# Kernel tuning notes

Measured on AMD Instinct MI355X. Metric: run time of the kernel, lower is better.

Reference implementation:

```python
import jax, jax.numpy as jnp
import numpy as np

IDIM = 512
HDIM = 1024
CDIM = 128  # part_size; topk uses k = 2*CDIM (share=True)
B, T = 16, 4096


def _multihot(idx, n):
    """idx: [B, T, K] int32 -> [B, T, n] float 0/1 multi-hot.
    Matches one_hot(idx, n).float().sum(-2); topk indices are unique so add==set."""
    b, t, k = idx.shape
    rows = jnp.arange(b * t)[:, None]
    m = jnp.zeros((b * t, n), jnp.float32).at[rows, idx.reshape(-1, k)].add(1.0)
    return m.reshape(b, t, n)


def setup_inputs() -> dict:
    key = jax.random.key(0)
    ks = jax.random.split(key, 12)
    inp = {}
    inp["x"] = jax.random.normal(ks[0], (B, T, IDIM), jnp.float32)
    inp["mask_prev"] = (jax.random.uniform(ks[1], (B, T, HDIM)) < 0.1).astype(jnp.float32)

    def lin(k, i, o):
        return jax.random.normal(k, (i, o), jnp.float32) * (1.0 / np.sqrt(i))

    dims_e = [IDIM, 512, 512, 512, HDIM]
    dims_d = [HDIM, 512, 512, 512, IDIM]
    for i in range(4):
        inp[f"e_w{i}"] = lin(ks[2 + i], dims_e[i], dims_e[i + 1])
        inp[f"e_b{i}"] = jnp.zeros((dims_e[i + 1],), jnp.float32)
        inp[f"d_w{i}"] = lin(ks[6 + i], dims_d[i], dims_d[i + 1])
        inp[f"d_b{i}"] = jnp.zeros((dims_d[i + 1],), jnp.float32)
    return inp


def _mlp(x, ws, bs):
    for w, b in zip(ws[:-1], bs[:-1]):
        x = jax.nn.relu(x @ w + b)
    return x @ ws[-1] + bs[-1]


def reference(x, mask_prev,
              e_w0, e_b0, e_w1, e_b1, e_w2, e_b2, e_w3, e_b3,
              d_w0, d_b0, d_w1, d_b1, d_w2, d_b2, d_w3, d_b3):
    h = _mlp(x, [e_w0, e_w1, e_w2, e_w3], [e_b0, e_b1, e_b2, e_b3])  # [B,T,HDIM]

    # hidden_exclude_activation (mask_prev is not None branch)
    h = jnp.where(mask_prev > 0, jnp.float32(0.0), h)  # h[mask_prev.byte()] = 0
    energy = h * h
    _, idx = jax.lax.top_k(energy, 2 * CDIM)            # sorted desc, like torch.topk
    mask_cur_share = _multihot(idx, HDIM)               # top 2*cdim multi-hot
    # h.masked_fill(~mask_cur_share, 0): keep only the shared top-2*cdim energies
    h = h * mask_cur_share

    # decoder
    out = _mlp(h, [d_w0, d_w1, d_w2, d_w3], [d_b0, d_b1, d_b2, d_b3])  # [B,T,IDIM]
    return out
```

## Files before the change

### kernel.cpp

```cpp
#include <hip/hip_runtime.h>

constexpr int NTOK  = 16 * 4096;
constexpr int KSEL  = 256;
constexpr int UCAP  = 8192;
constexpr int NCHNK = 2;
constexpr int UCAPT = UCAP * NCHNK;

using short8 = __attribute__((ext_vector_type(8))) short;
using ush4   = __attribute__((ext_vector_type(4))) unsigned short;
using f32x4  = __attribute__((ext_vector_type(4))) float;

__device__ inline unsigned short bf16_rne(float x) {
    unsigned u = __float_as_uint(x);
    unsigned r = u + 0x7fffu + ((u >> 16) & 1u);
    return (unsigned short)(r >> 16);
}
__device__ inline float bf16_f32(unsigned short h) {
    return __uint_as_float((unsigned)h << 16);
}

__device__ inline void gload_lds16(const unsigned short* g, unsigned short* l) {
    __builtin_amdgcn_global_load_lds(
        (const __attribute__((address_space(1))) void*)g,
        (__attribute__((address_space(3))) void*)l, 16, 0, 0);
}

__global__ __launch_bounds__(256)
void wsplit_t(const float* __restrict__ W, unsigned short* __restrict__ WhT,
              unsigned short* __restrict__ WlT, int K, int M)
{
    __shared__ float tile[32][33];
    const int tid = threadIdx.x;
    const int tx = tid & 31, ty = tid >> 5;
    const int m0 = blockIdx.x * 32, k0 = blockIdx.y * 32;
#pragma unroll
    for (int i = 0; i < 4; ++i)
        tile[ty + 8 * i][tx] = W[(size_t)(k0 + ty + 8 * i) * M + m0 + tx];
    __syncthreads();
#pragma unroll
    for (int i = 0; i < 4; ++i) {
        int m = ty + 8 * i;
        float v = tile[tx][m];
        unsigned short hh = bf16_rne(v);
        unsigned short ll = bf16_rne(v - bf16_f32(hh));
        WhT[(size_t)(m0 + m) * K + k0 + tx] = hh;
        WlT[(size_t)(m0 + m) * K + k0 + tx] = ll;
    }
}

template<int K, int RELU, int OUT_SPLIT>
__global__ __launch_bounds__(256)
void gemm_s(const unsigned short* __restrict__ A,
            const unsigned short* __restrict__ WhT,
            const unsigned short* __restrict__ WlT,
            const float* __restrict__ bias,
            void* Cp, int M, const float* __restrict__ mask)
{
    __shared__ __align__(16) unsigned short sAh[128 * 32];
    __shared__ __align__(16) unsigned short sAl[128 * 32];
    __shared__ __align__(16) unsigned short sBh[128 * 32];
    __shared__ __align__(16) unsigned short sBl[128 * 32];

    const int tid = threadIdx.x;
    const int lane = tid & 63, wid = tid >> 6;
    const int quad = lane >> 4, l16 = lane & 15;

    const int gridX = gridDim.x;
    int nwg = gridX * gridDim.y;
    int bid = blockIdx.y * gridX + blockIdx.x;
    int cpx = nwg >> 3;
    int swz = (bid & 7) * cpx + (bid >> 3);
    const int rowBase = (swz / gridX) * 128;
    const int colBase = (swz % gridX) * 128;

    const int wr = (wid & 1) * 64, wc = (wid >> 1) * 64;

    const int srl = lane >> 2;
    const int sq  = lane & 3;

    f32x4 acc[4][4];
#pragma unroll
    for (int i = 0; i < 4; ++i)
#pragma unroll
        for (int j = 0; j < 4; ++j)
            acc[i][j] = (f32x4){0.f, 0.f, 0.f, 0.f};

    for (int k0 = 0; k0 < K; k0 += 32) {
        __syncthreads();
#pragma unroll
        for (int i16 = 0; i16 < 2; ++i16) {
            const int row = wid * 32 + i16 * 16 + srl;
            const int qs = sq ^ ((row >> 1) & 3);
            const unsigned short* gAh = A  + (size_t)(rowBase + row) * (2 * K) + k0 + qs * 8;
            const unsigned short* gBh = WhT + (size_t)(colBase + row) * K + k0 + qs * 8;
            const unsigned short* gBl = WlT + (size_t)(colBase + row) * K + k0 + qs * 8;
            unsigned short* dst = (unsigned short*)0;
            const int dbase = (wid * 32 + i16 * 16) * 32;
            gload_lds16(gAh,     &sAh[dbase]);
            gload_lds16(gAh + K, &sAl[dbase]);
            gload_lds16(gBh,     &sBh[dbase]);
            gload_lds16(gBl,     &sBl[dbase]);
            (void)dst;
        }
        asm volatile("s_waitcnt vmcnt(0)" ::: "memory");
        __syncthreads();

        short8 ah[4], al[4], bh[4], bl[4];
#pragma unroll
        for (int t4 = 0; t4 < 4; ++t4) {
            const int ra = wr + t4 * 16 + l16;
            const int rb = wc + t4 * 16 + l16;
            const int ca = (quad ^ ((ra >> 1) & 3)) * 8;
            const int cb = (quad ^ ((rb >> 1) & 3)) * 8;
            ah[t4] = *(const short8*)&sAh[ra * 32 + ca];
            al[t4] = *(const short8*)&sAl[ra * 32 + ca];
            bh[t4] = *(const short8*)&sBh[rb * 32 + cb];
            bl[t4] = *(const short8*)&sBl[rb * 32 + cb];
        }
#pragma unroll
        for (int rt = 0; rt < 4; ++rt)
#pragma unroll
            for (int ct = 0; ct < 4; ++ct) {
                acc[rt][ct] = __builtin_amdgcn_mfma_f32_16x16x32_bf16(ah[rt], bh[ct], acc[rt][ct], 0, 0, 0);
                acc[rt][ct] = __builtin_amdgcn_mfma_f32_16x16x32_bf16(al[rt], bh[ct], acc[rt][ct], 0, 0, 0);
                acc[rt][ct] = __builtin_amdgcn_mfma_f32_16x16x32_bf16(ah[rt], bl[ct], acc[rt][ct], 0, 0, 0);
            }
    }

#pragma unroll
    for (int ct = 0; ct < 4; ++ct) {
        int col = colBase + wc + ct * 16 + l16;
        float bc = bias[col];
#pragma unroll
        for (int rt = 0; rt < 4; ++rt)
#pragma unroll
            for (int r = 0; r < 4; ++r) {
                int row = rowBase + wr + rt * 16 + quad * 4 + r;
                float v = acc[rt][ct][r] + bc;
                if (RELU) v = fmaxf(v, 0.f);
                if (mask) { if (mask[(size_t)row * M + col] > 0.f) v = 0.f; }
                if constexpr (OUT_SPLIT) {
                    unsigned short* Cs = (unsigned short*)Cp;
                    unsigned short hh = bf16_rne(v);
                    unsigned short ll = bf16_rne(v - bf16_f32(hh));
                    Cs[(size_t)row * (2 * M) + col]     = hh;
                    Cs[(size_t)row * (2 * M) + M + col] = ll;
                } else {
                    ((float*)Cp)[(size_t)row * M + col] = v;
                }
            }
    }
}

template<int K, int RELU, int OUT_SPLIT>
__global__ __launch_bounds__(256)
void gemm_u(const float* __restrict__ Af, const unsigned short* __restrict__ WhT,
            const unsigned short* __restrict__ WlT, const float* __restrict__ bias,
            void* Cp, int M, const float* __restrict__ mask)
{
    __shared__ __align__(16) unsigned short sAh[128 * 40];
    __shared__ __align__(16) unsigned short sAl[128 * 40];
    __shared__ __align__(16) unsigned short sBh[128 * 40];
    __shared__ __align__(16) unsigned short sBl[128 * 40];

    const int tid = threadIdx.x;
    const int lane = tid & 63, wid = tid >> 6;
    const int quad = lane >> 4, l16 = lane & 15;

    const int gridX = gridDim.x;
    int nwg = gridX * gridDim.y;
    int bid = blockIdx.y * gridX + blockIdx.x;
    int cpx = nwg >> 3;
    int swz = (bid & 7) * cpx + (bid >> 3);
    const int rowBase = (swz / gridX) * 128;
    const int colBase = (swz % gridX) * 128;

    const int wr = (wid & 1) * 64, wc = (wid >> 1) * 64;
    const int sr = tid >> 1;
    const int sk = (tid & 1) * 16;

    f32x4 acc[4][4];
#pragma unroll
    for (int i = 0; i < 4; ++i)
#pragma unroll
        for (int j = 0; j < 4; ++j)
            acc[i][j] = (f32x4){0.f, 0.f, 0.f, 0.f};

    for (int k0 = 0; k0 < K; k0 += 32) {
        const float* ap = &Af[(size_t)(rowBase + sr) * K + k0 + sk];
        float4 a0 = *(const float4*)ap;
        float4 a1 = *(const float4*)(ap + 4);
        float4 a2 = *(const float4*)(ap + 8);
        float4 a3 = *(const float4*)(ap + 12);
        const unsigned short* whp = &WhT[(size_t)(colBase + sr) * K + k0 + sk];
        const unsigned short* wlp = &WlT[(size_t)(colBase + sr) * K + k0 + sk];
        short8 wh0 = *(const short8*)whp;
        short8 wh1 = *(const short8*)(whp + 8);
        short8 wl0 = *(const short8*)wlp;
        short8 wl1 = *(const short8*)(wlp + 8);

        float f[16] = {a0.x, a0.y, a0.z, a0.w, a1.x, a1.y, a1.z, a1.w,
                       a2.x, a2.y, a2.z, a2.w, a3.x, a3.y, a3.z, a3.w};
        unsigned short __align__(16) hs[16], ls[16];
#pragma unroll
        for (int j = 0; j < 16; ++j) {
            hs[j] = bf16_rne(f[j]);
            ls[j] = bf16_rne(f[j] - bf16_f32(hs[j]));
        }

        __syncthreads();
        *(short8*)&sAh[sr * 40 + sk]     = *(short8*)&hs[0];
        *(short8*)&sAh[sr * 40 + sk + 8] = *(short8*)&hs[8];
        *(short8*)&sAl[sr * 40 + sk]     = *(short8*)&ls[0];
        *(short8*)&sAl[sr * 40 + sk + 8] = *(short8*)&ls[8];
        *(short8*)&sBh[sr * 40 + sk]     = wh0;
        *(short8*)&sBh[sr * 40 + sk + 8] = wh1;
        *(short8*)&sBl[sr * 40 + sk]     = wl0;
        *(short8*)&sBl[sr * 40 + sk + 8] = wl1;
        __syncthreads();

        short8 ah[4], al[4], bh[4], bl[4];
#pragma unroll
        for (int t4 = 0; t4 < 4; ++t4) {
            ah[t4] = *(const short8*)&sAh[(wr + t4 * 16 + l16) * 40 + quad * 8];
            al[t4] = *(const short8*)&sAl[(wr + t4 * 16 + l16) * 40 + quad * 8];
            bh[t4] = *(const short8*)&sBh[(wc + t4 * 16 + l16) * 40 + quad * 8];
            bl[t4] = *(const short8*)&sBl[(wc + t4 * 16 + l16) * 40 + quad * 8];
        }
#pragma unroll
        for (int rt = 0; rt < 4; ++rt)
#pragma unroll
            for (int ct = 0; ct < 4; ++ct) {
                acc[rt][ct] = __builtin_amdgcn_mfma_f32_16x16x32_bf16(ah[rt], bh[ct], acc[rt][ct], 0, 0, 0);
                acc[rt][ct] = __builtin_amdgcn_mfma_f32_16x16x32_bf16(al[rt], bh[ct], acc[rt][ct], 0, 0, 0);
                acc[rt][ct] = __builtin_amdgcn_mfma_f32_16x16x32_bf16(ah[rt], bl[ct], acc[rt][ct], 0, 0, 0);
            }
    }

#pragma unroll
    for (int ct = 0; ct < 4; ++ct) {
        int col = colBase + wc + ct * 16 + l16;
        float bc = bias[col];
#pragma unroll
        for (int rt = 0; rt < 4; ++rt)
#pragma unroll
            for (int r = 0; r < 4; ++r) {
                int row = rowBase + wr + rt * 16 + quad * 4 + r;
                float v = acc[rt][ct][r] + bc;
                if (RELU) v = fmaxf(v, 0.f);
                if (mask) { if (mask[(size_t)row * M + col] > 0.f) v = 0.f; }
                if constexpr (OUT_SPLIT) {
                    unsigned short* Cs = (unsigned short*)Cp;
                    unsigned short hh = bf16_rne(v);
                    unsigned short ll = bf16_rne(v - bf16_f32(hh));
                    Cs[(size_t)row * (2 * M) + col]     = hh;
                    Cs[(size_t)row * (2 * M) + M + col] = ll;
                } else {
                    ((float*)Cp)[(size_t)row * M + col] = v;
                }
            }
    }
}

__global__ __launch_bounds__(256)
void topk_pass1(const float* h, unsigned short* hsplit, int* __restrict__ meta)
{
    const int t = blockIdx.x, tid = threadIdx.x;
    const int lane = tid & 63, wid = tid >> 6;

    __shared__ unsigned hist[256];
    __shared__ unsigned wsum[4];
    __shared__ unsigned dmx[4];
    __shared__ unsigned s_prefix;
    __shared__ int s_need;

    float4 hv = ((const float4*)(h + (size_t)t * 1024))[tid];
    float v[4] = {hv.x, hv.y, hv.z, hv.w};
    unsigned u[4];
#pragma unroll
    for (int j = 0; j < 4; ++j) u[j] = __float_as_uint(v[j] * v[j]);

    if (tid == 0) { s_prefix = 0u; s_need = KSEL; }
    __syncthreads();

    for (int p = 3; p >= 0; --p) {
        unsigned pref = s_prefix;
        int need = s_need;
        hist[tid] = 0u;
        __syncthreads();
#pragma unroll
        for (int j = 0; j < 4; ++j) {
            bool match = (p == 3) || ((u[j] >> (8 * (p + 1))) == (pref >> (8 * (p + 1))));
            if (match) atomicAdd(&hist[(u[j] >> (8 * p)) & 255u], 1u);
        }
        __syncthreads();
        unsigned x = hist[tid];
        unsigned s = x;
#pragma unroll
        for (int off = 1; off < 64; off <<= 1) {
            unsigned o = __shfl_down(s, off);
            if (lane + off < 64) s += o;
        }
        if (lane == 0) wsum[wid] = s;
        __syncthreads();
        unsigned above = 0;
        for (int w = wid + 1; w < 4; ++w) above += wsum[w];
        unsigned incl = s + above;
        unsigned excl = incl - x;
        if (incl >= (unsigned)need && excl < (unsigned)need) {
            s_prefix = pref | ((unsigned)tid << (8 * p));
            s_need = need - (int)excl;
        }
        __syncthreads();
    }
    const unsigned tau = s_prefix;

    unsigned cg = 0, ce = 0;
#pragma unroll
    for (int j = 0; j < 4; ++j) {
        cg += (u[j] > tau) ? 1u : 0u;
        ce += (u[j] == tau) ? 1u : 0u;
    }
    unsigned packed = (cg << 16) | ce;
    unsigned ps = packed;
#pragma unroll
    for (int off = 1; off < 64; off <<= 1) {
        unsigned o = __shfl_up(ps, off);
        if (lane >= off) ps += o;
    }
    if (lane == 63) wsum[wid] = ps;
    __syncthreads();
    unsigned below = 0;
    for (int w = 0; w < wid; ++w) below += wsum[w];
    unsigned total = wsum[0] + wsum[1] + wsum[2] + wsum[3];
    unsigned incl = ps + below;
    int need_eq = KSEL - (int)(total >> 16);
    int eq_base = (int)((incl - packed) & 0xffffu);

    bool kp[4];
    {
        int r = 0;
#pragma unroll
        for (int j = 0; j < 4; ++j) {
            if (u[j] > tau) kp[j] = true;
            else if (u[j] == tau) { kp[j] = (eq_base + r) < need_eq; ++r; }
            else kp[j] = false;
        }
    }

    unsigned dmax = 0;
#pragma unroll
    for (int j = 0; j < 4; ++j) if (!kp[j] && u[j] > dmax) dmax = u[j];
#pragma unroll
    for (int off = 32; off > 0; off >>= 1) {
        unsigned o = __shfl_xor(dmax, off);
        if (o > dmax) dmax = o;
    }
    if (lane == 0) dmx[wid] = dmax;
    __syncthreads();
    if (tid == 0) {
        unsigned lo = dmx[0];
        for (int w = 1; w < 4; ++w) if (dmx[w] > lo) lo = dmx[w];
        float tauf = __uint_as_float(tau);
        float lof  = __uint_as_float(lo);
        if (tauf - lof <= fmaf(tauf, 4e-4f, 4e-5f)) {
            int slot = atomicAdd(&meta[0], 1);
            if (slot < UCAPT) meta[1 + slot] = t;
        }
    }

    unsigned short hs[4], ls[4];
#pragma unroll
    for (int j = 0; j < 4; ++j) {
        float ov = kp[j] ? v[j] : 0.f;
        hs[j] = bf16_rne(ov);
        ls[j] = bf16_rne(ov - bf16_f32(hs[j]));
    }
    size_t base = (size_t)t * 2048 + 4 * tid;
    *(ush4*)&hsplit[base]        = (ush4){hs[0], hs[1], hs[2], hs[3]};
    *(ush4*)&hsplit[base + 1024] = (ush4){ls[0], ls[1], ls[2], ls[3]};
}

__global__ __launch_bounds__(256)
void gather_x(const float* __restrict__ x, double* __restrict__ a64,
              const int* __restrict__ meta, int chunk)
{
    int cnt = meta[0]; if (cnt > UCAPT) cnt = UCAPT;
    int g = chunk * UCAP + blockIdx.x;
    if (g >= cnt) return;
    int tok = meta[1 + g];
    const float* src = &x[(size_t)tok * 512];
    double* dst = &a64[(size_t)blockIdx.x * 512];
    for (int i = threadIdx.x; i < 512; i += 256) dst[i] = (double)src[i];
}

template<int K, int RELU, int MASKED>
__global__ __launch_bounds__(256)
void gemm_f64(const double* __restrict__ A, const float* __restrict__ W,
              const float* __restrict__ bias, double* __restrict__ Cd,
              int M, const int* __restrict__ meta, const float* __restrict__ mp,
              int chunk)
{
    int cnt = meta[0]; if (cnt > UCAPT) cnt = UCAPT;
    int cloc = cnt - chunk * UCAP;
    if (cloc < 0) cloc = 0; if (cloc > UCAP) cloc = UCAP;
    const int rowBase = blockIdx.y * 64;
    if (rowBase >= cloc) return;
    const int colBase = blockIdx.x * 64;

    __shared__ double sA[16][65];
    __shared__ double sW[16][65];
    const int tid = threadIdx.x;
    const int tx = tid & 15, ty = tid >> 4;
    const int lr = tid & 63;
    const int lk4 = (tid >> 6) * 4;
    const int wk = tid >> 4;
    const int wc = (tid & 15) * 4;

    double acc[4][4] = {};

    for (int k0 = 0; k0 < K; k0 += 16) {
        const double* ap = &A[(size_t)(rowBase + lr) * K + k0 + lk4];
        double a0 = ap[0], a1 = ap[1], a2 = ap[2], a3 = ap[3];
        float4 wv = *(const float4*)&W[(size_t)(k0 + wk) * M + colBase + wc];
        __syncthreads();
        sA[lk4 + 0][lr] = a0; sA[lk4 + 1][lr] = a1;
        sA[lk4 + 2][lr] = a2; sA[lk4 + 3][lr] = a3;
        sW[wk][wc + 0] = (double)wv.x; sW[wk][wc + 1] = (double)wv.y;
        sW[wk][wc + 2] = (double)wv.z; sW[wk][wc + 3] = (double)wv.w;
        __syncthreads();
#pragma unroll
        for (int k = 0; k < 16; ++k) {
            double av[4], wl[4];
#pragma unroll
            for (int i = 0; i < 4; ++i) av[i] = sA[k][ty * 4 + i];
#pragma unroll
            for (int i = 0; i < 4; ++i) wl[i] = sW[k][tx * 4 + i];
#pragma unroll
            for (int a = 0; a < 4; ++a)
#pragma unroll
                for (int b = 0; b < 4; ++b)
                    acc[a][b] = fma(av[a], wl[b], acc[a][b]);
        }
    }

#pragma unroll
    for (int a = 0; a < 4; ++a) {
        int row = rowBase + ty * 4 + a;
        if (row >= cloc) continue;
        int tok = MASKED ? meta[1 + chunk * UCAP + row] : 0;
#pragma unroll
        for (int b = 0; b < 4; ++b) {
            int col = colBase + tx * 4 + b;
            double vv = acc[a][b] + (double)bias[col];
            if (RELU) vv = vv > 0.0 ? vv : 0.0;
            if (MASKED) { if (mp[(size_t)tok * 1024 + col] > 0.f) vv = 0.0; }
            Cd[(size_t)row * M + col] = vv;
        }
    }
}

__global__ __launch_bounds__(256)
void topk_pass2(const double* __restrict__ h64, unsigned short* __restrict__ hsplit,
                const int* __restrict__ meta, int chunk)
{
    int cnt = meta[0]; if (cnt > UCAPT) cnt = UCAPT;
    int g = chunk * UCAP + blockIdx.x;
    if (g >= cnt) return;
    int tok = meta[1 + g];

    __shared__ double se[1024];
    __shared__ unsigned short si[1024];
    __shared__ unsigned char keep[1024];
    const int tid = threadIdx.x;
    const double* row = &h64[(size_t)blockIdx.x * 1024];

#pragma unroll
    for (int t = 0; t < 4; ++t) {
        int i = tid + t * 256;
        double v = row[i];
        se[i] = v * v;
        si[i] = (unsigned short)i;
        keep[i] = 0;
    }
    __syncthreads();

    for (int ksz = 2; ksz <= 1024; ksz <<= 1) {
        for (int j = ksz >> 1; j > 0; j >>= 1) {
#pragma unroll
            for (int t = 0; t < 4; ++t) {
                int i = tid + t * 256;
                int p = i ^ j;
                if (p > i) {
                    double ei = se[i], ep = se[p];
                    unsigned short ii = si[i], ip = si[p];
                    bool later = !((ei > ep) || (ei == ep && ii < ip));
                    bool dir = ((i & ksz) == 0);
                    if (later == dir) {
                        se[i] = ep; se[p] = ei;
                        si[i] = ip; si[p] = ii;
                    }
                }
            }
            __syncthreads();
        }
    }

    keep[si[tid]] = 1;
    __syncthreads();

#pragma unroll
    for (int t = 0; t < 4; ++t) {
        int i = tid + t * 256;
        float vv = keep[i] ? (float)row[i] : 0.f;
        unsigned short hh = bf16_rne(vv);
        unsigned short ll = bf16_rne(vv - bf16_f32(hh));
        hsplit[(size_t)tok * 2048 + i]        = hh;
        hsplit[(size_t)tok * 2048 + 1024 + i] = ll;
    }
}

extern "C" void kernel_launch(void* const* d_in, const int* in_sizes, int n_in,
                              void* d_out, int out_size, void* d_ws, size_t ws_size,
                              hipStream_t stream)
{
    (void)n_in; (void)out_size; (void)ws_size;

    const float* x  = (const float*)d_in[0];
    const float* mp = (const float*)d_in[1];

    const float *ew[4], *eb[4], *dw[4], *db[4];
    bool interleaved = (in_sizes[4] == 1024 * 512);
    for (int i = 0; i < 4; ++i) {
        if (interleaved) {
            ew[i] = (const float*)d_in[2 + 4 * i];
            eb[i] = (const float*)d_in[3 + 4 * i];
            dw[i] = (const float*)d_in[4 + 4 * i];
            db[i] = (const float*)d_in[5 + 4 * i];
        } else {
            ew[i] = (const float*)d_in[2 + 2 * i];
            eb[i] = (const float*)d_in[3 + 2 * i];
            dw[i] = (const float*)d_in[10 + 2 * i];
            db[i] = (const float*)d_in[11 + 2 * i];
        }
    }

    char* ws = (char*)d_ws;
    char* ob = (char*)d_out;
    const size_t MB = 1024 * 1024;

    unsigned short* S1 = (unsigned short*)(ws);
    unsigned short* S2 = (unsigned short*)(ws + 128 * MB);
    unsigned short* S3 = (unsigned short*)(ws + 256 * MB);
    float*          hF = (float*)(ws);
    unsigned short* Hs = (unsigned short*)(ws);
    unsigned short* D1 = (unsigned short*)(ws + 256 * MB);
    unsigned short* D2 = (unsigned short*)(ws);
    unsigned short* D3 = (unsigned short*)(ws + 128 * MB);
    float*          out = (float*)d_out;

    unsigned short* p0 = (unsigned short*)ob;
    unsigned short* EW0h = p0 + 0;        unsigned short* EW0l = p0 + 262144;
    unsigned short* EW1h = p0 + 524288;   unsigned short* EW1l = p0 + 786432;
    unsigned short* EW2h = p0 + 1048576;  unsigned short* EW2l = p0 + 1310720;
    unsigned short* EW3h = p0 + 1572864;  unsigned short* EW3l = p0 + 2097152;
    unsigned short* W0h  = p0 + 2621440;  unsigned short* W0l  = p0 + 3145728;
    unsigned short* W1h  = p0 + 3670016;  unsigned short* W1l  = p0 + 3932160;
    unsigned short* W2h  = p0 + 4194304;  unsigned short* W2l  = p0 + 4456448;
    int* meta = (int*)(ob + 16 * MB);

    unsigned short* W3h = (unsigned short*)(ws + 256 * MB);
    unsigned short* W3l = W3h + 262144;

    double* a64 = (double*)(ws + 256 * MB);
    double* b64 = (double*)(ws + 288 * MB);
    double* h64 = (double*)(ws + 320 * MB);

    dim3 blk(256);

    wsplit_t<<<dim3(16, 16), blk, 0, stream>>>(ew[0], EW0h, EW0l, 512, 512);
    wsplit_t<<<dim3(16, 16), blk, 0, stream>>>(ew[1], EW1h, EW1l, 512, 512);
    wsplit_t<<<dim3(16, 16), blk, 0, stream>>>(ew[2], EW2h, EW2l, 512, 512);
    wsplit_t<<<dim3(32, 16), blk, 0, stream>>>(ew[3], EW3h, EW3l, 512, 1024);
    wsplit_t<<<dim3(16, 32), blk, 0, stream>>>(dw[0], W0h,  W0l,  1024, 512);
    wsplit_t<<<dim3(16, 16), blk, 0, stream>>>(dw[1], W1h,  W1l,  512, 512);
    wsplit_t<<<dim3(16, 16), blk, 0, stream>>>(dw[2], W2h,  W2l,  512, 512);
    hipMemsetAsync(meta, 0, sizeof(int), stream);

    dim3 ge(4, NTOK / 128), ge4(8, NTOK / 128);
    gemm_u<512, 1, 1><<<ge,  blk, 0, stream>>>(x,  EW0h, EW0l, eb[0], S1, 512,  nullptr);
    gemm_s<512, 1, 1><<<ge,  blk, 0, stream>>>(S1, EW1h, EW1l, eb[1], S2, 512,  nullptr);
    gemm_s<512, 1, 1><<<ge,  blk, 0, stream>>>(S2, EW2h, EW2l, eb[2], S3, 512,  nullptr);
    gemm_s<512, 0, 0><<<ge4, blk, 0, stream>>>(S3, EW3h, EW3l, eb[3], hF, 1024, mp);

    topk_pass1<<<dim3(NTOK), blk, 0, stream>>>(hF, Hs, meta);

    dim3 g64a(8, UCAP / 64), g64b(16, UCAP / 64);
    for (int c = 0; c < NCHNK; ++c) {
        gather_x<<<dim3(UCAP), blk, 0, stream>>>(x, a64, meta, c);
        gemm_f64<512, 1, 0><<<g64a, blk, 0, stream>>>(a64, ew[0], eb[0], b64, 512,  meta, nullptr, c);
        gemm_f64<512, 1, 0><<<g64a, blk, 0, stream>>>(b64, ew[1], eb[1], a64, 512,  meta, nullptr, c);
        gemm_f64<512, 1, 0><<<g64a, blk, 0, stream>>>(a64, ew[2], eb[2], b64, 512,  meta, nullptr, c);
        gemm_f64<512, 0, 1><<<g64b, blk, 0, stream>>>(b64, ew[3], eb[3], h64, 1024, meta, mp, c);
        topk_pass2<<<dim3(UCAP), blk, 0, stream>>>(h64, Hs, meta, c);
    }

    dim3 gd(4, NTOK / 128);
    gemm_s<1024, 1, 1><<<gd, blk, 0, stream>>>(Hs, W0h, W0l, db[0], D1, 512, nullptr);
    gemm_s<512, 1, 1><<<gd, blk, 0, stream>>>(D1, W1h, W1l, db[1], D2, 512, nullptr);
    wsplit_t<<<dim3(16, 16), blk, 0, stream>>>(dw[3], W3h, W3l, 512, 512);
    gemm_s<512, 1, 1><<<gd, blk, 0, stream>>>(D2, W2h, W2l, db[2], D3, 512, nullptr);
    gemm_s<512, 0, 0><<<gd, blk, 0, stream>>>(D3, W3h, W3l, db[3], out, 512, nullptr);
}
```

Baseline: 3.998 ms.

## Double-buffer LDS tiles in split-bf16 GEMM to overlap loads with MFMA

```diff
diff --git a/kernel.cpp b/kernel.cpp
--- a/kernel.cpp
+++ b/kernel.cpp
@@ -56,10 +56,10 @@
             const float* __restrict__ bias,
             void* Cp, int M, const float* __restrict__ mask)
 {
-    __shared__ __align__(16) unsigned short sAh[128 * 32];
-    __shared__ __align__(16) unsigned short sAl[128 * 32];
-    __shared__ __align__(16) unsigned short sBh[128 * 32];
-    __shared__ __align__(16) unsigned short sBl[128 * 32];
+    __shared__ __align__(16) unsigned short sAh[2][128 * 32];
+    __shared__ __align__(16) unsigned short sAl[2][128 * 32];
+    __shared__ __align__(16) unsigned short sBh[2][128 * 32];
+    __shared__ __align__(16) unsigned short sBl[2][128 * 32];
 
     const int tid = threadIdx.x;
     const int lane = tid & 63, wid = tid >> 6;
@@ -85,25 +85,31 @@
         for (int j = 0; j < 4; ++j)
             acc[i][j] = (f32x4){0.f, 0.f, 0.f, 0.f};
 
-    for (int k0 = 0; k0 < K; k0 += 32) {
-        __syncthreads();
+    auto STAGE = [&](int k0, int b) {
 #pragma unroll
         for (int i16 = 0; i16 < 2; ++i16) {
             const int row = wid * 32 + i16 * 16 + srl;
             const int qs = sq ^ ((row >> 1) & 3);
-            const unsigned short* gAh = A  + (size_t)(rowBase + row) * (2 * K) + k0 + qs * 8;
+            const unsigned short* gA  = A   + (size_t)(rowBase + row) * (2 * K) + k0 + qs * 8;
             const unsigned short* gBh = WhT + (size_t)(colBase + row) * K + k0 + qs * 8;
             const unsigned short* gBl = WlT + (size_t)(colBase + row) * K + k0 + qs * 8;
-            unsigned short* dst = (unsigned short*)0;
             const int dbase = (wid * 32 + i16 * 16) * 32;
-            gload_lds16(gAh,     &sAh[dbase]);
-            gload_lds16(gAh + K, &sAl[dbase]);
-            gload_lds16(gBh,     &sBh[dbase]);
-            gload_lds16(gBl,     &sBl[dbase]);
-            (void)dst;
-        }
-        asm volatile("s_waitcnt vmcnt(0)" ::: "memory");
-        __syncthreads();
+            gload_lds16(gA,     &sAh[b][dbase]);
+            gload_lds16(gA + K, &sAl[b][dbase]);
+            gload_lds16(gBh,    &sBh[b][dbase]);
+            gload_lds16(gBl,    &sBl[b][dbase]);
+        }
+    };
+
+    constexpr int NT = K / 32;
+
+    STAGE(0, 0);
+    asm volatile("s_waitcnt vmcnt(0)" ::: "memory");
+    __syncthreads();
+
+    for (int t = 0; t < NT; ++t) {
+        const int cur = t & 1;
+        if (t + 1 < NT) STAGE((t + 1) * 32, cur ^ 1);
 
         short8 ah[4], al[4], bh[4], bl[4];
 #pragma unroll
@@ -112,10 +118,10 @@
             const int rb = wc + t4 * 16 + l16;
             const int ca = (quad ^ ((ra >> 1) & 3)) * 8;
             const int cb = (quad ^ ((rb >> 1) & 3)) * 8;
-            ah[t4] = *(const short8*)&sAh[ra * 32 + ca];
-            al[t4] = *(const short8*)&sAl[ra * 32 + ca];
-            bh[t4] = *(const short8*)&sBh[rb * 32 + cb];
-            bl[t4] = *(const short8*)&sBl[rb * 32 + cb];
+            ah[t4] = *(const short8*)&sAh[cur][ra * 32 + ca];
+            al[t4] = *(const short8*)&sAl[cur][ra * 32 + ca];
+            bh[t4] = *(const short8*)&sBh[cur][rb * 32 + cb];
+            bl[t4] = *(const short8*)&sBl[cur][rb * 32 + cb];
         }
 #pragma unroll
         for (int rt = 0; rt < 4; ++rt)
@@ -125,6 +131,9 @@
                 acc[rt][ct] = __builtin_amdgcn_mfma_f32_16x16x32_bf16(al[rt], bh[ct], acc[rt][ct], 0, 0, 0);
                 acc[rt][ct] = __builtin_amdgcn_mfma_f32_16x16x32_bf16(ah[rt], bl[ct], acc[rt][ct], 0, 0, 0);
             }
+
+        asm volatile("s_waitcnt vmcnt(0)" ::: "memory");
+        __syncthreads();
     }
 
 #pragma unroll
```

Result: slower. 4.218 ms (+5.5%).

## Widen GEMM tiles, stage split-bf16 epilogue via LDS, bitpack mask, drop fp32 hidden

Applied to the files above, without the earlier changes.

```diff
diff --git a/kernel.cpp b/kernel.cpp
--- a/kernel.cpp
+++ b/kernel.cpp
@@ -23,6 +23,20 @@
     __builtin_amdgcn_global_load_lds(
         (const __attribute__((address_space(1))) void*)g,
         (__attribute__((address_space(3))) void*)l, 16, 0, 0);
+}
+
+__global__ __launch_bounds__(256)
+void mask_pack(const float* __restrict__ mp, unsigned long long* __restrict__ mb)
+{
+    const int lane = threadIdx.x & 63;
+    size_t w = ((size_t)blockIdx.x * blockDim.x + threadIdx.x) >> 6;
+    size_t nw = ((size_t)gridDim.x * blockDim.x) >> 6;
+    const size_t total = (size_t)NTOK * 1024 / 64;
+    for (; w < total; w += nw) {
+        float v = mp[w * 64 + lane];
+        unsigned long long b = __ballot(v > 0.f);
+        if (lane == 0) mb[w] = b;
+    }
 }
 
 __global__ __launch_bounds__(256)
@@ -54,12 +68,13 @@
             const unsigned short* __restrict__ WhT,
             const unsigned short* __restrict__ WlT,
             const float* __restrict__ bias,
-            void* Cp, int M, const float* __restrict__ mask)
-{
-    __shared__ __align__(16) unsigned short sAh[128 * 32];
-    __shared__ __align__(16) unsigned short sAl[128 * 32];
-    __shared__ __align__(16) unsigned short sBh[128 * 32];
-    __shared__ __align__(16) unsigned short sBl[128 * 32];
+            void* Cp, int M, const unsigned* __restrict__ mbits)
+{
+    __shared__ __align__(16) unsigned short sMem[24576];
+    unsigned short* sAh = sMem;
+    unsigned short* sAl = sMem + 4096;
+    unsigned short* sBh = sMem + 8192;
+    unsigned short* sBl = sMem + 16384;
 
     const int tid = threadIdx.x;
     const int lane = tid & 63, wid = tid >> 6;
@@ -71,18 +86,17 @@
     int cpx = nwg >> 3;
     int swz = (bid & 7) * cpx + (bid >> 3);
     const int rowBase = (swz / gridX) * 128;
-    const int colBase = (swz % gridX) * 128;
-
-    const int wr = (wid & 1) * 64, wc = (wid >> 1) * 64;
-
-    const int srl = lane >> 2;
-    const int sq  = lane & 3;
-
-    f32x4 acc[4][4];
+    const int colBase = (swz % gridX) * 256;
+
+    const int wr = (wid & 1) * 64;
+    const int wc = (wid >> 1) * 128;
+    const int srl = lane >> 2, sq = lane & 3;
+
+    f32x4 acc[4][8];
 #pragma unroll
     for (int i = 0; i < 4; ++i)
 #pragma unroll
-        for (int j = 0; j < 4; ++j)
+        for (int j = 0; j < 8; ++j)
             acc[i][j] = (f32x4){0.f, 0.f, 0.f, 0.f};
 
     for (int k0 = 0; k0 < K; k0 += 32) {
@@ -91,77 +105,117 @@
         for (int i16 = 0; i16 < 2; ++i16) {
             const int row = wid * 32 + i16 * 16 + srl;
             const int qs = sq ^ ((row >> 1) & 3);
-            const unsigned short* gAh = A  + (size_t)(rowBase + row) * (2 * K) + k0 + qs * 8;
+            const unsigned short* gA = A + (size_t)(rowBase + row) * (2 * K) + k0 + qs * 8;
+            const int dbase = (wid * 32 + i16 * 16) * 32;
+            gload_lds16(gA,     sAh + dbase);
+            gload_lds16(gA + K, sAl + dbase);
+        }
+#pragma unroll
+        for (int i16 = 0; i16 < 4; ++i16) {
+            const int row = wid * 64 + i16 * 16 + srl;
+            const int qs = sq ^ ((row >> 1) & 3);
             const unsigned short* gBh = WhT + (size_t)(colBase + row) * K + k0 + qs * 8;
             const unsigned short* gBl = WlT + (size_t)(colBase + row) * K + k0 + qs * 8;
-            unsigned short* dst = (unsigned short*)0;
-            const int dbase = (wid * 32 + i16 * 16) * 32;
-            gload_lds16(gAh,     &sAh[dbase]);
-            gload_lds16(gAh + K, &sAl[dbase]);
-            gload_lds16(gBh,     &sBh[dbase]);
-            gload_lds16(gBl,     &sBl[dbase]);
-            (void)dst;
+            const int dbase = (wid * 64 + i16 * 16) * 32;
+            gload_lds16(gBh, sBh + dbase);
+            gload_lds16(gBl, sBl + dbase);
         }
         asm volatile("s_waitcnt vmcnt(0)" ::: "memory");
         __syncthreads();
 
-        short8 ah[4], al[4], bh[4], bl[4];
+        short8 ah[4], al[4];
 #pragma unroll
         for (int t4 = 0; t4 < 4; ++t4) {
             const int ra = wr + t4 * 16 + l16;
-            const int rb = wc + t4 * 16 + l16;
             const int ca = (quad ^ ((ra >> 1) & 3)) * 8;
-            const int cb = (quad ^ ((rb >> 1) & 3)) * 8;
             ah[t4] = *(const short8*)&sAh[ra * 32 + ca];
             al[t4] = *(const short8*)&sAl[ra * 32 + ca];
-            bh[t4] = *(const short8*)&sBh[rb * 32 + cb];
-            bl[t4] = *(const short8*)&sBl[rb * 32 + cb];
-        }
-#pragma unroll
-        for (int rt = 0; rt < 4; ++rt)
-#pragma unroll
-            for (int ct = 0; ct < 4; ++ct) {
-                acc[rt][ct] = __builtin_amdgcn_mfma_f32_16x16x32_bf16(ah[rt], bh[ct], acc[rt][ct], 0, 0, 0);
-                acc[rt][ct] = __builtin_amdgcn_mfma_f32_16x16x32_bf16(al[rt], bh[ct], acc[rt][ct], 0, 0, 0);
-                acc[rt][ct] = __builtin_amdgcn_mfma_f32_16x16x32_bf16(ah[rt], bl[ct], acc[rt][ct], 0, 0, 0);
+        }
+#pragma unroll
+        for (int ct = 0; ct < 8; ++ct) {
+            const int rb = wc + ct * 16 + l16;
+            const int cb = (quad ^ ((rb >> 1) & 3)) * 8;
+            short8 bh = *(const short8*)&sBh[rb * 32 + cb];
+            short8 bl = *(const short8*)&sBl[rb * 32 + cb];
+#pragma unroll
+            for (int rt = 0; rt < 4; ++rt) {
+                acc[rt][ct] = __builtin_amdgcn_mfma_f32_16x16x32_bf16(ah[rt], bh, acc[rt][ct], 0, 0, 0);
+                acc[rt][ct] = __builtin_amdgcn_mfma_f32_16x16x32_bf16(al[rt], bh, acc[rt][ct], 0, 0, 0);
+                acc[rt][ct] = __builtin_amdgcn_mfma_f32_16x16x32_bf16(ah[rt], bl, acc[rt][ct], 0, 0, 0);
             }
-    }
-
-#pragma unroll
-    for (int ct = 0; ct < 4; ++ct) {
-        int col = colBase + wc + ct * 16 + l16;
-        float bc = bias[col];
-#pragma unroll
-        for (int rt = 0; rt < 4; ++rt)
-#pragma unroll
-            for (int r = 0; r < 4; ++r) {
-                int row = rowBase + wr + rt * 16 + quad * 4 + r;
-                float v = acc[rt][ct][r] + bc;
-                if (RELU) v = fmaxf(v, 0.f);
-                if (mask) { if (mask[(size_t)row * M + col] > 0.f) v = 0.f; }
-                if constexpr (OUT_SPLIT) {
-                    unsigned short* Cs = (unsigned short*)Cp;
-                    unsigned short hh = bf16_rne(v);
-                    unsigned short ll = bf16_rne(v - bf16_f32(hh));
-                    Cs[(size_t)row * (2 * M) + col]     = hh;
-                    Cs[(size_t)row * (2 * M) + M + col] = ll;
-                } else {
-                    ((float*)Cp)[(size_t)row * M + col] = v;
+        }
+    }
+
+    float bcv[8];
+#pragma unroll
+    for (int ct = 0; ct < 8; ++ct) bcv[ct] = bias[colBase + wc + ct * 16 + l16];
+
+    if constexpr (OUT_SPLIT) {
+        unsigned short* Cs = (unsigned short*)Cp;
+        for (int cg = 0; cg < 2; ++cg) {
+            for (int half = 0; half < 2; ++half) {
+                __syncthreads();
+                if ((wid >> 1) == cg) {
+#pragma unroll
+                    for (int ct = 0; ct < 8; ++ct)
+#pragma unroll
+                        for (int rt = 0; rt < 4; ++rt)
+#pragma unroll
+                            for (int r = 0; r < 4; ++r) {
+                                int rowL = wr + rt * 16 + quad * 4 + r;
+                                int colL = ct * 16 + l16;
+                                float v = acc[rt][ct][r] + bcv[ct];
+                                if (RELU) v = fmaxf(v, 0.f);
+                                if (mbits) {
+                                    int colg = colBase + wc + ct * 16 + l16;
+                                    unsigned wbit = mbits[(size_t)(rowBase + rowL) * (M >> 5) + (colg >> 5)];
+                                    if ((wbit >> (colg & 31)) & 1u) v = 0.f;
+                                }
+                                unsigned short hh = bf16_rne(v);
+                                unsigned short ov = half ? bf16_rne(v - bf16_f32(hh)) : hh;
+                                sMem[rowL * 136 + colL] = ov;
+                            }
+                }
+                __syncthreads();
+#pragma unroll
+                for (int j = 0; j < 8; ++j) {
+                    int row = (tid >> 2) + ((j & 1) << 6);
+                    int ch  = (tid & 3) + ((j >> 1) << 2);
+                    short8 vv = *(const short8*)&sMem[row * 136 + ch * 8];
+                    *(short8*)&Cs[(size_t)(rowBase + row) * (2 * M) + (size_t)half * M
+                                  + colBase + cg * 128 + ch * 8] = vv;
                 }
             }
-    }
-}
-
-template<int K, int RELU, int OUT_SPLIT>
+        }
+    } else {
+        float* Cf = (float*)Cp;
+#pragma unroll
+        for (int ct = 0; ct < 8; ++ct) {
+            int col = colBase + wc + ct * 16 + l16;
+#pragma unroll
+            for (int rt = 0; rt < 4; ++rt)
+#pragma unroll
+                for (int r = 0; r < 4; ++r) {
+                    int row = rowBase + wr + rt * 16 + quad * 4 + r;
+                    float v = acc[rt][ct][r] + bcv[ct];
+                    if (RELU) v = fmaxf(v, 0.f);
+                    Cf[(size_t)row * M + col] = v;
+                }
+        }
+    }
+}
+
+template<int K, int RELU>
 __global__ __launch_bounds__(256)
 void gemm_u(const float* __restrict__ Af, const unsigned short* __restrict__ WhT,
             const unsigned short* __restrict__ WlT, const float* __restrict__ bias,
-            void* Cp, int M, const float* __restrict__ mask)
-{
-    __shared__ __align__(16) unsigned short sAh[128 * 40];
-    __shared__ __align__(16) unsigned short sAl[128 * 40];
-    __shared__ __align__(16) unsigned short sBh[128 * 40];
-    __shared__ __align__(16) unsigned short sBl[128 * 40];
+            void* Cp, int M)
+{
+    __shared__ __align__(16) unsigned short sMem[20480];
+    unsigned short* sAh = sMem;
+    unsigned short* sAl = sMem + 5120;
+    unsigned short* sBh = sMem + 10240;
+    unsigned short* sBl = sMem + 15360;
 
     const int tid = threadIdx.x;
     const int lane = tid & 63, wid = tid >> 6;
@@ -237,33 +291,41 @@
             }
     }
 
-#pragma unroll
-    for (int ct = 0; ct < 4; ++ct) {
-        int col = colBase + wc + ct * 16 + l16;
-        float bc = bias[col];
-#pragma unroll
-        for (int rt = 0; rt < 4; ++rt)
-#pragma unroll
-            for (int r = 0; r < 4; ++r) {
-                int row = rowBase + wr + rt * 16 + quad * 4 + r;
-                float v = acc[rt][ct][r] + bc;
-                if (RELU) v = fmaxf(v, 0.f);
-                if (mask) { if (mask[(size_t)row * M + col] > 0.f) v = 0.f; }
-                if constexpr (OUT_SPLIT) {
-                    unsigned short* Cs = (unsigned short*)Cp;
+    float bcv[4];
+#pragma unroll
+    for (int ct = 0; ct < 4; ++ct) bcv[ct] = bias[colBase + wc + ct * 16 + l16];
+
+    unsigned short* Cs = (unsigned short*)Cp;
+    for (int half = 0; half < 2; ++half) {
+        __syncthreads();
+#pragma unroll
+        for (int ct = 0; ct < 4; ++ct)
+#pragma unroll
+            for (int rt = 0; rt < 4; ++rt)
+#pragma unroll
+                for (int r = 0; r < 4; ++r) {
+                    int rowL = wr + rt * 16 + quad * 4 + r;
+                    int colL = wc + ct * 16 + l16;
+                    float v = acc[rt][ct][r] + bcv[ct];
+                    if (RELU) v = fmaxf(v, 0.f);
                     unsigned short hh = bf16_rne(v);
-                    unsigned short ll = bf16_rne(v - bf16_f32(hh));
-                    Cs[(size_t)row * (2 * M) + col]     = hh;
-                    Cs[(size_t)row * (2 * M) + M + col] = ll;
-                } else {
-                    ((float*)Cp)[(size_t)row * M + col] = v;
+                    unsigned short ov = half ? bf16_rne(v - bf16_f32(hh)) : hh;
+                    sMem[rowL * 136 + colL] = ov;
                 }
-            }
-    }
-}
-
-__global__ __launch_bounds__(256)
-void topk_pass1(const float* h, unsigned short* hsplit, int* __restrict__ meta)
+        __syncthreads();
+#pragma unroll
+        for (int j = 0; j < 8; ++j) {
+            int row = (tid >> 2) + ((j & 1) << 6);
+            int ch  = (tid & 3) + ((j >> 1) << 2);
+            short8 vv = *(const short8*)&sMem[row * 136 + ch * 8];
+            *(short8*)&Cs[(size_t)(rowBase + row) * (2 * M) + (size_t)half * M
+                          + colBase + ch * 8] = vv;
+        }
+    }
+}
+
+__global__ __launch_bounds__(256)
+void topk_pass1(unsigned short* hsplit, int* __restrict__ meta)
 {
     const int t = blockIdx.x, tid = threadIdx.x;
     const int lane = tid & 63, wid = tid >> 6;
@@ -274,11 +336,16 @@
     __shared__ unsigned s_prefix;
     __shared__ int s_need;
 
-    float4 hv = ((const float4*)(h + (size_t)t * 1024))[tid];
-    float v[4] = {hv.x, hv.y, hv.z, hv.w};
+    unsigned short* hr = hsplit + (size_t)t * 2048;
+    ush4 hv = *(const ush4*)&hr[4 * tid];
+    ush4 lv = *(const ush4*)&hr[1024 + 4 * tid];
+    float v[4];
     unsigned u[4];
 #pragma unroll
-    for (int j = 0; j < 4; ++j) u[j] = __float_as_uint(v[j] * v[j]);
+    for (int j = 0; j < 4; ++j) {
+        v[j] = bf16_f32(hv[j]) + bf16_f32(lv[j]);
+        u[j] = __float_as_uint(v[j] * v[j]);
+    }
 
     if (tid == 0) { s_prefix = 0u; s_need = KSEL; }
     __syncthreads();
@@ -369,16 +436,14 @@
         }
     }
 
-    unsigned short hs[4], ls[4];
+    ush4 ho, lo4;
 #pragma unroll
     for (int j = 0; j < 4; ++j) {
-        float ov = kp[j] ? v[j] : 0.f;
-        hs[j] = bf16_rne(ov);
-        ls[j] = bf16_rne(ov - bf16_f32(hs[j]));
-    }
-    size_t base = (size_t)t * 2048 + 4 * tid;
-    *(ush4*)&hsplit[base]        = (ush4){hs[0], hs[1], hs[2], hs[3]};
-    *(ush4*)&hsplit[base + 1024] = (ush4){ls[0], ls[1], ls[2], ls[3]};
+        ho[j]  = kp[j] ? hv[j] : (unsigned short)0;
+        lo4[j] = kp[j] ? lv[j] : (unsigned short)0;
+    }
+    *(ush4*)&hr[4 * tid]        = ho;
+    *(ush4*)&hr[1024 + 4 * tid] = lo4;
 }
 
 __global__ __launch_bounds__(256)
@@ -552,7 +617,6 @@
     unsigned short* S1 = (unsigned short*)(ws);
     unsigned short* S2 = (unsigned short*)(ws + 128 * MB);
     unsigned short* S3 = (unsigned short*)(ws + 256 * MB);
-    float*          hF = (float*)(ws);
     unsigned short* Hs = (unsigned short*)(ws);
     unsigned short* D1 = (unsigned short*)(ws + 256 * MB);
     unsigned short* D2 = (unsigned short*)(ws);
@@ -568,6 +632,8 @@
     unsigned short* W1h  = p0 + 3670016;  unsigned short* W1l  = p0 + 3932160;
     unsigned short* W2h  = p0 + 4194304;  unsigned short* W2l  = p0 + 4456448;
     int* meta = (int*)(ob + 16 * MB);
+    unsigned long long* mbits64 = (unsigned long long*)(ob + 17 * MB);
+    const unsigned* mbitsu = (const unsigned*)mbits64;
 
     unsigned short* W3h = (unsigned short*)(ws + 256 * MB);
     unsigned short* W3l = W3h + 262144;
@@ -586,14 +652,17 @@
     wsplit_t<<<dim3(16, 16), blk, 0, stream>>>(dw[1], W1h,  W1l,  512, 512);
     wsplit_t<<<dim3(16, 16), blk, 0, stream>>>(dw[2], W2h,  W2l,  512, 512);
     hipMemsetAsync(meta, 0, sizeof(int), stream);
-
-    dim3 ge(4, NTOK / 128), ge4(8, NTOK / 128);
-    gemm_u<512, 1, 1><<<ge,  blk, 0, stream>>>(x,  EW0h, EW0l, eb[0], S1, 512,  nullptr);
-    gemm_s<512, 1, 1><<<ge,  blk, 0, stream>>>(S1, EW1h, EW1l, eb[1], S2, 512,  nullptr);
-    gemm_s<512, 1, 1><<<ge,  blk, 0, stream>>>(S2, EW2h, EW2l, eb[2], S3, 512,  nullptr);
-    gemm_s<512, 0, 0><<<ge4, blk, 0, stream>>>(S3, EW3h, EW3l, eb[3], hF, 1024, mp);
-
-    topk_pass1<<<dim3(NTOK), blk, 0, stream>>>(hF, Hs, meta);
+    mask_pack<<<dim3(2048), blk, 0, stream>>>(mp, mbits64);
+
+    dim3 geu(4, NTOK / 128);
+    dim3 ge2(2, NTOK / 128);
+    dim3 ge4c(4, NTOK / 128);
+    gemm_u<512, 1><<<geu, blk, 0, stream>>>(x,  EW0h, EW0l, eb[0], S1, 512);
+    gemm_s<512, 1, 1><<<ge2,  blk, 0, stream>>>(S1, EW1h, EW1l, eb[1], S2, 512,  nullptr);
+    gemm_s<512, 1, 1><<<ge2,  blk, 0, stream>>>(S2, EW2h, EW2l, eb[2], S3, 512,  nullptr);
+    gemm_s<512, 0, 1><<<ge4c, blk, 0, stream>>>(S3, EW3h, EW3l, eb[3], Hs, 1024, mbitsu);
+
+    topk_pass1<<<dim3(NTOK), blk, 0, stream>>>(Hs, meta);
 
     dim3 g64a(8, UCAP / 64), g64b(16, UCAP / 64);
     for (int c = 0; c < NCHNK; ++c) {
@@ -605,10 +674,9 @@
         topk_pass2<<<dim3(UCAP), blk, 0, stream>>>(h64, Hs, meta, c);
     }
 
-    dim3 gd(4, NTOK / 128);
-    gemm_s<1024, 1, 1><<<gd, blk, 0, stream>>>(Hs, W0h, W0l, db[0], D1, 512, nullptr);
-    gemm_s<512, 1, 1><<<gd, blk, 0, stream>>>(D1, W1h, W1l, db[1], D2, 512, nullptr);
+    gemm_s<1024, 1, 1><<<ge2, blk, 0, stream>>>(Hs, W0h, W0l, db[0], D1, 512, nullptr);
+    gemm_s<512, 1, 1><<<ge2, blk, 0, stream>>>(D1, W1h, W1l, db[1], D2, 512, nullptr);
     wsplit_t<<<dim3(16, 16), blk, 0, stream>>>(dw[3], W3h, W3l, 512, 512);
-    gemm_s<512, 1, 1><<<gd, blk, 0, stream>>>(D2, W2h, W2l, db[2], D3, 512, nullptr);
-    gemm_s<512, 0, 0><<<gd, blk, 0, stream>>>(D3, W3h, W3l, db[3], out, 512, nullptr);
-}
+    gemm_s<512, 1, 1><<<ge2, blk, 0, stream>>>(D2, W2h, W2l, db[2], D3, 512, nullptr);
+    gemm_s<512, 0, 0><<<ge2, blk, 0, stream>>>(D3, W3h, W3l, db[3], out, 512, nullptr);
+}
```

Result: slower. 4.875 ms (+22.0%).
